# Optimization experiments

Measured on AMD Instinct MI355X. Metric: run time of the kernel, lower is better.

Reference implementation:

```python
import jax, jax.numpy as jnp
import numpy as np
import math

B, S, D, H = 4, 2048, 1024, 16
DK = D // H


def setup_inputs() -> dict:
    key = jax.random.key(0)
    ks = jax.random.split(key, 10)
    scale = 0.02
    q = jax.random.normal(ks[0], (B, S, D), jnp.float32)
    k = jax.random.normal(ks[1], (B, S, D), jnp.float32)
    v = jax.random.normal(ks[2], (B, S, D), jnp.float32)
    # additive float src_mask [S,S]: causal-style mask (0 allowed, -1e9 blocked)
    causal = jnp.tril(jnp.ones((S, S), jnp.float32))
    src_mask = jnp.where(causal > 0, 0.0, -1e9).astype(jnp.float32)
    # key padding mask [B,S]: last 256 keys of each sequence are padding
    key_padding_mask = (jnp.arange(S)[None, :] >= (S - 256)) & jnp.ones((B, 1), bool)
    Wq = jax.random.normal(ks[3], (D, D), jnp.float32) * scale
    Wk = jax.random.normal(ks[4], (D, D), jnp.float32) * scale
    Wv = jax.random.normal(ks[5], (D, D), jnp.float32) * scale
    Wo = jax.random.normal(ks[6], (D, D), jnp.float32) * scale
    bq = jnp.zeros((D,), jnp.float32)
    bk = jnp.zeros((D,), jnp.float32)
    bv = jnp.zeros((D,), jnp.float32)
    bo = jnp.zeros((D,), jnp.float32)
    return {"q": q, "k": k, "v": v, "src_mask": src_mask,
            "key_padding_mask": key_padding_mask,
            "Wq": Wq, "bq": bq, "Wk": Wk, "bk": bk,
            "Wv": Wv, "bv": bv, "Wo": Wo, "bo": bo}


def reference(q, k, v, src_mask, key_padding_mask, Wq, bq, Wk, bk, Wv, bv, Wo, bo):
    bs = q.shape[0]
    # torch Linear: x @ W.T + b
    qh = (q @ Wq.T + bq).reshape(bs, -1, H, DK).transpose(0, 2, 1, 3)  # [B,H,S,dk]
    kh = (k @ Wk.T + bk).reshape(bs, -1, H, DK).transpose(0, 2, 1, 3)
    vh = (v @ Wv.T + bv).reshape(bs, -1, H, DK).transpose(0, 2, 1, 3)
    scores = jnp.einsum('bhqd,bhkd->bhqk', qh, kh) / math.sqrt(DK)
    # float additive src_mask: scores += mask[None, None]
    scores = scores + src_mask[None, None, :, :]
    # boolean key padding mask: fill masked keys with -inf
    scores = jnp.where(key_padding_mask[:, None, None, :], -jnp.inf, scores)
    attn = jax.nn.softmax(scores, axis=-1)  # dropout inactive (eval / p=0)
    out = jnp.einsum('bhqk,bhkd->bhqd', attn, vh)
    concat = out.transpose(0, 2, 1, 3).reshape(bs, -1, D)
    return concat @ Wo.T + bo
```

## Files before the change

### kernel.cpp

```cpp
#include <hip/hip_runtime.h>
#include <hip/hip_bf16.h>
#include <stdint.h>

#define S_LEN 2048
#define DMODEL 1024
#define DKH 64
#define KV_ALLOWED 1792
#define QSCALE 0.18033688011112042f

typedef __attribute__((ext_vector_type(4))) float f32x4;
typedef __attribute__((ext_vector_type(8))) short bf16x8;
typedef __attribute__((ext_vector_type(8))) unsigned short u16x8;
typedef __attribute__((ext_vector_type(4))) unsigned short u16x4;

static __device__ __forceinline__ float fast_exp2(float x) {
    return __builtin_amdgcn_exp2f(x);
}
static __device__ __forceinline__ unsigned short f2bf(float f) {
    __hip_bfloat16 h = __float2bfloat16(f);
    union { __hip_bfloat16 h; unsigned short u; } c; c.h = h; return c.u;
}
static __device__ __forceinline__ float bf2f(unsigned short b) {
    union { unsigned u; float f; } c; c.u = ((unsigned)b) << 16; return c.f;
}
static __device__ __forceinline__ u16x8 cvt2x4(const float4 a, const float4 b) {
    u16x8 r;
    r[0] = f2bf(a.x); r[1] = f2bf(a.y); r[2] = f2bf(a.z); r[3] = f2bf(a.w);
    r[4] = f2bf(b.x); r[5] = f2bf(b.y); r[6] = f2bf(b.z); r[7] = f2bf(b.w);
    return r;
}

#define BAR_LGKM() do { \
    asm volatile("s_waitcnt lgkmcnt(0)" ::: "memory"); \
    __builtin_amdgcn_s_barrier(); \
    __builtin_amdgcn_sched_barrier(0); \
} while (0)

#define A_OFF(buf) ((buf) * 8192)
#define B_OFF(buf) (16384 + (buf) * 16384)

__global__ __launch_bounds__(256) void cvt_w(
        const float* __restrict__ w0, const float* __restrict__ w1,
        const float* __restrict__ w2, const float* __restrict__ w3,
        unsigned short* __restrict__ out) {
    const float* src = (blockIdx.y == 0) ? w0 : (blockIdx.y == 1) ? w1
                     : (blockIdx.y == 2) ? w2 : w3;
    unsigned short* dst = out + (size_t)blockIdx.y * 1048576;
    const int i = (blockIdx.x * 256 + threadIdx.x) * 16;
    float4 f0 = *(const float4*)(src + i);
    float4 f1 = *(const float4*)(src + i + 4);
    float4 f2 = *(const float4*)(src + i + 8);
    float4 f3 = *(const float4*)(src + i + 12);
    *(u16x8*)(dst + i)     = cvt2x4(f0, f1);
    *(u16x8*)(dst + i + 8) = cvt2x4(f2, f3);
}

template<int OUT_MODE>
__global__ __launch_bounds__(512) void gemm_proj(
        const float* __restrict__ A, const unsigned short* __restrict__ Bw,
        const float* __restrict__ bias, unsigned short* __restrict__ Cout) {
    __shared__ unsigned short smem[49152];
    const int tid = threadIdx.x;
    const int lane = tid & 63, wv = tid >> 6;
    const int wr = wv >> 2, wc = wv & 3;
    const int g = lane >> 4, lo = lane & 15;
    const int wg = ((int)blockIdx.x & 7) * 32 + ((int)blockIdx.x >> 3);
    const int m0 = (wg >> 2) << 7, n0 = (wg & 3) << 8;

    const int sr = tid >> 2;
    const int sc = (tid & 3) << 4;
    const int swzA = (sr & 7) << 3;
    const int gsw = ((lane & 7) ^ (lane >> 3)) << 3;
    const int rswz = (lo & 7) << 3;

    f32x4 acc[4][4];
#pragma unroll
    for (int i = 0; i < 4; ++i)
#pragma unroll
        for (int j = 0; j < 4; ++j) acc[i][j] = (f32x4){0.f, 0.f, 0.f, 0.f};

    const float* gaBase = A + (size_t)(m0 + sr) * 1024 + sc;

    auto LOADA = [&](int ko, float4* pa) {
        const float* ga = gaBase + ko;
        pa[0] = *(const float4*)(ga);      pa[1] = *(const float4*)(ga + 4);
        pa[2] = *(const float4*)(ga + 8);  pa[3] = *(const float4*)(ga + 12);
    };
    auto WRITEA = [&](int buf, const float4* pa) {
        *(u16x8*)&smem[A_OFF(buf) + sr * 64 + ((sc + 0) ^ swzA)] = cvt2x4(pa[0], pa[1]);
        *(u16x8*)&smem[A_OFF(buf) + sr * 64 + ((sc + 8) ^ swzA)] = cvt2x4(pa[2], pa[3]);
    };
    auto LOADB = [&](int ko, u16x8* pb) {
#pragma unroll
        for (int c = 0; c < 4; ++c) {
            const int rb = c * 64 + wv * 8 + (lane >> 3);
            pb[c] = *(const u16x8*)(Bw + (size_t)(n0 + rb) * 1024 + ko + gsw);
        }
    };
    auto WRITEB = [&](int buf, const u16x8* pb) {
#pragma unroll
        for (int c = 0; c < 4; ++c) {
            const int rb = c * 64 + wv * 8 + (lane >> 3);
            *(u16x8*)&smem[B_OFF(buf) + rb * 64 + ((lane & 7) << 3)] = pb[c];
        }
    };

    float4 pa[4];
    u16x8 pb[4];
    LOADA(0, pa);  LOADB(0, pb);
    WRITEA(0, pa); WRITEB(0, pb);
    LOADA(64, pa); LOADB(64, pb);
    BAR_LGKM();

    int cur = 0;
    for (int k0 = 0; k0 < 1024; k0 += 64) {
        if (k0 + 64 < 1024) {
            WRITEA(cur ^ 1, pa);
            WRITEB(cur ^ 1, pb);
        }
        __builtin_amdgcn_sched_barrier(0);
        const int ka = (k0 + 128 < 1024) ? (k0 + 128) : 0;
        LOADA(ka, pa);
        LOADB(ka, pb);
        __builtin_amdgcn_sched_barrier(0);

#pragma unroll
        for (int kk = 0; kk < 2; ++kk) {
            bf16x8 af[4], bfr[4];
#pragma unroll
            for (int mi = 0; mi < 4; ++mi) {
                const int r = wr * 64 + mi * 16 + lo;
                af[mi] = *(const bf16x8*)&smem[A_OFF(cur) + r * 64 + ((kk * 32 + g * 8) ^ rswz)];
            }
#pragma unroll
            for (int ni = 0; ni < 4; ++ni) {
                const int r = wc * 64 + ni * 16 + lo;
                bfr[ni] = *(const bf16x8*)&smem[B_OFF(cur) + r * 64 + ((kk * 32 + g * 8) ^ rswz)];
            }
#pragma unroll
            for (int mi = 0; mi < 4; ++mi)
#pragma unroll
                for (int ni = 0; ni < 4; ++ni)
                    acc[mi][ni] = __builtin_amdgcn_mfma_f32_16x16x32_bf16(af[mi], bfr[ni], acc[mi][ni], 0, 0, 0);
        }
        BAR_LGKM();
        cur ^= 1;
    }

    if (OUT_MODE == 2) {
#pragma unroll
        for (int mi = 0; mi < 4; ++mi) {
            const int rb = wr * 64 + mi * 16 + g * 4;
#pragma unroll
            for (int ni = 0; ni < 4; ++ni) {
                const int c = wc * 64 + ni * 16 + lo;
                const float bvv = bias[n0 + c];
                u16x4 w;
#pragma unroll
                for (int j = 0; j < 4; ++j) w[j] = f2bf(acc[mi][ni][j] + bvv);
                *(u16x4*)&smem[c * 128 + (rb ^ ((c & 15) << 3))] = w;
            }
        }
        __syncthreads();
        const int c2 = tid >> 1, hf = tid & 1;
        const int bglob = m0 >> 11;
        unsigned short* vrow = Cout + (((size_t)(bglob * 1024 + n0 + c2)) << 11)
                             + (m0 & 2047) + hf * 64;
#pragma unroll
        for (int i = 0; i < 8; ++i) {
            u16x8 vv = *(const u16x8*)&smem[c2 * 128 + ((hf * 64 + i * 8) ^ ((c2 & 15) << 3))];
            *(u16x8*)(vrow + i * 8) = vv;
        }
    } else {
#pragma unroll
        for (int mi = 0; mi < 4; ++mi) {
            const int row = m0 + wr * 64 + mi * 16 + g * 4;
#pragma unroll
            for (int ni = 0; ni < 4; ++ni) {
                const int col = n0 + wc * 64 + ni * 16 + lo;
                const float bvv = bias[col];
#pragma unroll
                for (int j = 0; j < 4; ++j)
                    Cout[(size_t)(row + j) * 1024 + col] = f2bf(acc[mi][ni][j] + bvv);
            }
        }
    }
}

__global__ __launch_bounds__(512) void gemm_out(
        const unsigned short* __restrict__ Ab, const unsigned short* __restrict__ Bw,
        const float* __restrict__ bias, float* __restrict__ Cout) {
    __shared__ unsigned short smem[49152];
    const int tid = threadIdx.x;
    const int lane = tid & 63, wv = tid >> 6;
    const int wr = wv >> 2, wc = wv & 3;
    const int g = lane >> 4, lo = lane & 15;
    const int wg = ((int)blockIdx.x & 7) * 32 + ((int)blockIdx.x >> 3);
    const int m0 = (wg >> 2) << 7, n0 = (wg & 3) << 8;
    const int gsw = ((lane & 7) ^ (lane >> 3)) << 3;
    const int rswz = (lo & 7) << 3;

    f32x4 acc[4][4];
#pragma unroll
    for (int i = 0; i < 4; ++i)
#pragma unroll
        for (int j = 0; j < 4; ++j) acc[i][j] = (f32x4){0.f, 0.f, 0.f, 0.f};

    auto LOADAB = [&](int ko, u16x8* pa, u16x8* pb) {
#pragma unroll
        for (int c = 0; c < 2; ++c) {
            const int rb = c * 64 + wv * 8 + (lane >> 3);
            pa[c] = *(const u16x8*)(Ab + (size_t)(m0 + rb) * 1024 + ko + gsw);
        }
#pragma unroll
        for (int c = 0; c < 4; ++c) {
            const int rb = c * 64 + wv * 8 + (lane >> 3);
            pb[c] = *(const u16x8*)(Bw + (size_t)(n0 + rb) * 1024 + ko + gsw);
        }
    };
    auto WRITEAB = [&](int buf, const u16x8* pa, const u16x8* pb) {
#pragma unroll
        for (int c = 0; c < 2; ++c) {
            const int rb = c * 64 + wv * 8 + (lane >> 3);
            *(u16x8*)&smem[A_OFF(buf) + rb * 64 + ((lane & 7) << 3)] = pa[c];
        }
#pragma unroll
        for (int c = 0; c < 4; ++c) {
            const int rb = c * 64 + wv * 8 + (lane >> 3);
            *(u16x8*)&smem[B_OFF(buf) + rb * 64 + ((lane & 7) << 3)] = pb[c];
        }
    };

    u16x8 pa[2], pb[4];
    LOADAB(0, pa, pb);
    WRITEAB(0, pa, pb);
    LOADAB(64, pa, pb);
    BAR_LGKM();

    int cur = 0;
    for (int k0 = 0; k0 < 1024; k0 += 64) {
        if (k0 + 64 < 1024) WRITEAB(cur ^ 1, pa, pb);
        __builtin_amdgcn_sched_barrier(0);
        const int ka = (k0 + 128 < 1024) ? (k0 + 128) : 0;
        LOADAB(ka, pa, pb);
        __builtin_amdgcn_sched_barrier(0);

#pragma unroll
        for (int kk = 0; kk < 2; ++kk) {
            bf16x8 af[4], bfr[4];
#pragma unroll
            for (int mi = 0; mi < 4; ++mi) {
                const int r = wr * 64 + mi * 16 + lo;
                af[mi] = *(const bf16x8*)&smem[A_OFF(cur) + r * 64 + ((kk * 32 + g * 8) ^ rswz)];
            }
#pragma unroll
            for (int ni = 0; ni < 4; ++ni) {
                const int r = wc * 64 + ni * 16 + lo;
                bfr[ni] = *(const bf16x8*)&smem[B_OFF(cur) + r * 64 + ((kk * 32 + g * 8) ^ rswz)];
            }
#pragma unroll
            for (int mi = 0; mi < 4; ++mi)
#pragma unroll
                for (int ni = 0; ni < 4; ++ni)
                    acc[mi][ni] = __builtin_amdgcn_mfma_f32_16x16x32_bf16(af[mi], bfr[ni], acc[mi][ni], 0, 0, 0);
        }
        BAR_LGKM();
        cur ^= 1;
    }

#pragma unroll
    for (int mi = 0; mi < 4; ++mi) {
        const int row = m0 + wr * 64 + mi * 16 + g * 4;
#pragma unroll
        for (int ni = 0; ni < 4; ++ni) {
            const int col = n0 + wc * 64 + ni * 16 + lo;
            const float bvv = bias[col];
#pragma unroll
            for (int j = 0; j < 4; ++j)
                Cout[(size_t)(row + j) * 1024 + col] = acc[mi][ni][j] + bvv;
        }
    }
}

__global__ __launch_bounds__(512) void attn_fwd(
        unsigned short* __restrict__ QO, const unsigned short* __restrict__ Kh,
        const unsigned short* __restrict__ Vt) {
    __shared__ unsigned short K_lds[64 * 72];
    __shared__ unsigned short Vt_lds[64 * 68];
    __shared__ unsigned short P_lds[8][16 * 68];

    const int bh = blockIdx.x;
    const int b = bh >> 4, h = bh & 15;
    const int yy = blockIdx.y;
    const int tid = threadIdx.x, lane = tid & 63, wv = tid >> 6;
    const int g = lane >> 4, lo = lane & 15;
    const int str = tid >> 3;
    const int stc = (tid & 7) << 3;

    const unsigned short* kbase = Kh + ((size_t)b * S_LEN + str) * DMODEL + h * DKH + stc;
    const unsigned short* vbase = Vt + ((size_t)(bh * 64 + str)) * S_LEN + stc;

    const int ytile = (wv < 4) ? (31 - yy) : yy;
    const int qw0 = (ytile << 6) + ((wv & 3) << 4);
    const int qrow = qw0 + lo;
    const int lastk = (qrow < KV_ALLOWED - 1) ? qrow : (KV_ALLOWED - 1);
    const int wmin_last = (qw0 < KV_ALLOWED - 1) ? qw0 : (KV_ALLOWED - 1);
    const int wave_last_k = (qw0 + 15 < KV_ALLOWED - 1) ? (qw0 + 15) : (KV_ALLOWED - 1);

    const int nt_long = (32 - yy < 28) ? (32 - yy) : 28;

    bf16x8 qf[2];
#pragma unroll
    for (int kk = 0; kk < 2; ++kk) {
        const u16x8 raw = *(const u16x8*)(QO + ((size_t)b * S_LEN + qrow) * DMODEL
                                          + h * DKH + kk * 32 + g * 8);
        bf16x8 sc16;
#pragma unroll
        for (int e = 0; e < 8; ++e) sc16[e] = (short)f2bf(bf2f(raw[e]) * QSCALE);
        qf[kk] = sc16;
    }

    float l_part = 0.f;
    f32x4 o_acc[4];
#pragma unroll
    for (int nf = 0; nf < 4; ++nf) o_acc[nf] = (f32x4){0.f, 0.f, 0.f, 0.f};

    u16x8 cK = *(const u16x8*)kbase;
    u16x8 cV = *(const u16x8*)vbase;

    for (int t = 0; t < nt_long; ++t) {
        const int kv0 = t << 6;
        __syncthreads();
        *(u16x8*)&K_lds[str * 72 + stc] = cK;
        *(u16x8*)&Vt_lds[str * 68 + stc] = cV;
        __syncthreads();
        if (t + 1 < nt_long) {
            cK = *(const u16x8*)(kbase + (size_t)(kv0 + 64) * DMODEL);
            cV = *(const u16x8*)(vbase + kv0 + 64);
        }

        if (kv0 <= wave_last_k) {
            f32x4 sacc[4];
#pragma unroll
            for (int nf = 0; nf < 4; ++nf) sacc[nf] = (f32x4){0.f, 0.f, 0.f, 0.f};
            __builtin_amdgcn_s_setprio(1);
#pragma unroll
            for (int kk = 0; kk < 2; ++kk) {
                bf16x8 kf[4];
#pragma unroll
                for (int nf = 0; nf < 4; ++nf)
                    kf[nf] = *(const bf16x8*)&K_lds[(nf * 16 + lo) * 72 + kk * 32 + g * 8];
#pragma unroll
                for (int nf = 0; nf < 4; ++nf)
                    sacc[nf] = __builtin_amdgcn_mfma_f32_16x16x32_bf16(kf[nf], qf[kk], sacc[nf], 0, 0, 0);
            }
            __builtin_amdgcn_s_setprio(0);

            if (kv0 + 63 > wmin_last) {
#pragma unroll
                for (int nf = 0; nf < 4; ++nf)
#pragma unroll
                    for (int j = 0; j < 4; ++j) {
                        const int col = kv0 + nf * 16 + g * 4 + j;
                        sacc[nf][j] = (col <= lastk) ? sacc[nf][j] : -__builtin_inff();
                    }
            }

            float ps[4];
#pragma unroll
            for (int nf = 0; nf < 4; ++nf) {
#pragma unroll
                for (int j = 0; j < 4; ++j)
                    sacc[nf][j] = fast_exp2(sacc[nf][j]);
                ps[nf] = (sacc[nf][0] + sacc[nf][1]) + (sacc[nf][2] + sacc[nf][3]);
            }
            l_part += (ps[0] + ps[1]) + (ps[2] + ps[3]);

#pragma unroll
            for (int nf = 0; nf < 4; ++nf) {
                u16x4 pk;
#pragma unroll
                for (int j = 0; j < 4; ++j) pk[j] = f2bf(sacc[nf][j]);
                *(u16x4*)&P_lds[wv][lo * 68 + nf * 16 + g * 4] = pk;
            }

            __builtin_amdgcn_s_setprio(1);
#pragma unroll
            for (int kk = 0; kk < 2; ++kk) {
                const bf16x8 pf = *(const bf16x8*)&P_lds[wv][lo * 68 + kk * 32 + g * 8];
                bf16x8 vf[4];
#pragma unroll
                for (int nf = 0; nf < 4; ++nf)
                    vf[nf] = *(const bf16x8*)&Vt_lds[(nf * 16 + lo) * 68 + kk * 32 + g * 8];
#pragma unroll
                for (int nf = 0; nf < 4; ++nf)
                    o_acc[nf] = __builtin_amdgcn_mfma_f32_16x16x32_bf16(vf[nf], pf, o_acc[nf], 0, 0, 0);
            }
            __builtin_amdgcn_s_setprio(0);
        }
    }

    float l_run = l_part + __shfl_xor(l_part, 16, 64);
    l_run += __shfl_xor(l_run, 32, 64);

    const float rl = 1.0f / l_run;
    unsigned short* orow = QO + ((size_t)b * S_LEN + qrow) * DMODEL + h * DKH;
#pragma unroll
    for (int nf = 0; nf < 4; ++nf) {
        u16x4 ok;
#pragma unroll
        for (int j = 0; j < 4; ++j) ok[j] = f2bf(o_acc[nf][j] * rl);
        *(u16x4*)(orow + nf * 16 + g * 4) = ok;
    }
}

extern "C" void kernel_launch(void* const* d_in, const int* in_sizes, int n_in,
                              void* d_out, int out_size, void* d_ws, size_t ws_size,
                              hipStream_t stream) {
    const float* q  = (const float*)d_in[0];
    const float* k  = (const float*)d_in[1];
    const float* v  = (const float*)d_in[2];
    const float* Wq = (const float*)d_in[5];
    const float* bq = (const float*)d_in[6];
    const float* Wk = (const float*)d_in[7];
    const float* bk = (const float*)d_in[8];
    const float* Wv = (const float*)d_in[9];
    const float* bv = (const float*)d_in[10];
    const float* Wo = (const float*)d_in[11];
    const float* bo = (const float*)d_in[12];

    unsigned short* ws = (unsigned short*)d_ws;
    unsigned short* qh = ws;
    unsigned short* kh = ws + 8388608;
    unsigned short* vt = ws + 16777216;
    unsigned short* Wb = ws + 25165824;

    cvt_w<<<dim3(256, 4), dim3(256), 0, stream>>>(Wq, Wk, Wv, Wo, Wb);

    gemm_proj<0><<<256, dim3(512), 0, stream>>>(q, Wb,           bq, qh);
    gemm_proj<0><<<256, dim3(512), 0, stream>>>(k, Wb + 1048576, bk, kh);
    gemm_proj<2><<<256, dim3(512), 0, stream>>>(v, Wb + 2097152, bv, vt);

    attn_fwd<<<dim3(64, 16), dim3(512), 0, stream>>>(qh, kh, vt);

    gemm_out<<<256, dim3(512), 0, stream>>>(qh, Wb + 3145728, bo, (float*)d_out);
}
```

Before: 172.4 us.

## Have each attention wave process two query tiles to reuse K/V fragments

The attention kernel drops from 8 waves to 4 waves per block. Each wave now handles both the long (31-yy) and short (yy) query tiles, sharing the K and V fragments it reads from LDS across the two. Staging loads double per thread to keep the 64x64 tiles filled. This halves LDS fragment reads per MFMA, but it raises register pressure and leaves fewer waves per block to hide latency.

New measurement: 188.9 us. 1.1x slower.

```diff
diff --git a/kernel.cpp b/kernel.cpp
--- a/kernel.cpp
+++ b/kernel.cpp
@@ -282,67 +282,90 @@
     }
 }
 
-__global__ __launch_bounds__(512) void attn_fwd(
+__global__ __launch_bounds__(256) void attn_fwd(
         unsigned short* __restrict__ QO, const unsigned short* __restrict__ Kh,
         const unsigned short* __restrict__ Vt) {
     __shared__ unsigned short K_lds[64 * 72];
     __shared__ unsigned short Vt_lds[64 * 68];
-    __shared__ unsigned short P_lds[8][16 * 68];
+    __shared__ unsigned short P_lds[4][2][16 * 68];
 
     const int bh = blockIdx.x;
     const int b = bh >> 4, h = bh & 15;
     const int yy = blockIdx.y;
     const int tid = threadIdx.x, lane = tid & 63, wv = tid >> 6;
     const int g = lane >> 4, lo = lane & 15;
-    const int str = tid >> 3;
-    const int stc = (tid & 7) << 3;
+    const int str = tid >> 2;
+    const int stc = (tid & 3) << 4;
 
     const unsigned short* kbase = Kh + ((size_t)b * S_LEN + str) * DMODEL + h * DKH + stc;
     const unsigned short* vbase = Vt + ((size_t)(bh * 64 + str)) * S_LEN + stc;
 
-    const int ytile = (wv < 4) ? (31 - yy) : yy;
-    const int qw0 = (ytile << 6) + ((wv & 3) << 4);
-    const int qrow = qw0 + lo;
-    const int lastk = (qrow < KV_ALLOWED - 1) ? qrow : (KV_ALLOWED - 1);
-    const int wmin_last = (qw0 < KV_ALLOWED - 1) ? qw0 : (KV_ALLOWED - 1);
-    const int wave_last_k = (qw0 + 15 < KV_ALLOWED - 1) ? (qw0 + 15) : (KV_ALLOWED - 1);
+    const int ytA = 31 - yy, ytB = yy;
+    const int qw0A = (ytA << 6) + (wv << 4);
+    const int qw0B = (ytB << 6) + (wv << 4);
+    const int qrowA = qw0A + lo, qrowB = qw0B + lo;
+    const int lastkA = (qrowA < KV_ALLOWED - 1) ? qrowA : (KV_ALLOWED - 1);
+    const int lastkB = (qrowB < KV_ALLOWED - 1) ? qrowB : (KV_ALLOWED - 1);
+    const int wminA = (qw0A < KV_ALLOWED - 1) ? qw0A : (KV_ALLOWED - 1);
+    const int wminB = (qw0B < KV_ALLOWED - 1) ? qw0B : (KV_ALLOWED - 1);
+    const int wlkA = (qw0A + 15 < KV_ALLOWED - 1) ? (qw0A + 15) : (KV_ALLOWED - 1);
+    const int wlkB = (qw0B + 15 < KV_ALLOWED - 1) ? (qw0B + 15) : (KV_ALLOWED - 1);
 
     const int nt_long = (32 - yy < 28) ? (32 - yy) : 28;
 
-    bf16x8 qf[2];
+    bf16x8 qfA[2], qfB[2];
 #pragma unroll
     for (int kk = 0; kk < 2; ++kk) {
-        const u16x8 raw = *(const u16x8*)(QO + ((size_t)b * S_LEN + qrow) * DMODEL
-                                          + h * DKH + kk * 32 + g * 8);
-        bf16x8 sc16;
-#pragma unroll
-        for (int e = 0; e < 8; ++e) sc16[e] = (short)f2bf(bf2f(raw[e]) * QSCALE);
-        qf[kk] = sc16;
-    }
-
-    float l_part = 0.f;
-    f32x4 o_acc[4];
-#pragma unroll
-    for (int nf = 0; nf < 4; ++nf) o_acc[nf] = (f32x4){0.f, 0.f, 0.f, 0.f};
-
-    u16x8 cK = *(const u16x8*)kbase;
-    u16x8 cV = *(const u16x8*)vbase;
+        const u16x8 rawA = *(const u16x8*)(QO + ((size_t)b * S_LEN + qrowA) * DMODEL
+                                           + h * DKH + kk * 32 + g * 8);
+        const u16x8 rawB = *(const u16x8*)(QO + ((size_t)b * S_LEN + qrowB) * DMODEL
+                                           + h * DKH + kk * 32 + g * 8);
+        bf16x8 sA, sB;
+#pragma unroll
+        for (int e = 0; e < 8; ++e) {
+            sA[e] = (short)f2bf(bf2f(rawA[e]) * QSCALE);
+            sB[e] = (short)f2bf(bf2f(rawB[e]) * QSCALE);
+        }
+        qfA[kk] = sA; qfB[kk] = sB;
+    }
+
+    float lpA = 0.f, lpB = 0.f;
+    f32x4 oA[4], oB[4];
+#pragma unroll
+    for (int nf = 0; nf < 4; ++nf) {
+        oA[nf] = (f32x4){0.f, 0.f, 0.f, 0.f};
+        oB[nf] = (f32x4){0.f, 0.f, 0.f, 0.f};
+    }
+
+    u16x8 cK0 = *(const u16x8*)kbase;
+    u16x8 cK1 = *(const u16x8*)(kbase + 8);
+    u16x8 cV0 = *(const u16x8*)vbase;
+    u16x8 cV1 = *(const u16x8*)(vbase + 8);
 
     for (int t = 0; t < nt_long; ++t) {
         const int kv0 = t << 6;
         __syncthreads();
-        *(u16x8*)&K_lds[str * 72 + stc] = cK;
-        *(u16x8*)&Vt_lds[str * 68 + stc] = cV;
+        *(u16x8*)&K_lds[str * 72 + stc] = cK0;
+        *(u16x8*)&K_lds[str * 72 + stc + 8] = cK1;
+        *(u16x8*)&Vt_lds[str * 68 + stc] = cV0;
+        *(u16x8*)&Vt_lds[str * 68 + stc + 8] = cV1;
         __syncthreads();
         if (t + 1 < nt_long) {
-            cK = *(const u16x8*)(kbase + (size_t)(kv0 + 64) * DMODEL);
-            cV = *(const u16x8*)(vbase + kv0 + 64);
-        }
-
-        if (kv0 <= wave_last_k) {
-            f32x4 sacc[4];
-#pragma unroll
-            for (int nf = 0; nf < 4; ++nf) sacc[nf] = (f32x4){0.f, 0.f, 0.f, 0.f};
+            cK0 = *(const u16x8*)(kbase + (size_t)(kv0 + 64) * DMODEL);
+            cK1 = *(const u16x8*)(kbase + (size_t)(kv0 + 64) * DMODEL + 8);
+            cV0 = *(const u16x8*)(vbase + kv0 + 64);
+            cV1 = *(const u16x8*)(vbase + kv0 + 64 + 8);
+        }
+
+        if (kv0 <= wlkA) {
+            const bool actB = (kv0 <= wlkB);
+
+            f32x4 sA[4], sB[4];
+#pragma unroll
+            for (int nf = 0; nf < 4; ++nf) {
+                sA[nf] = (f32x4){0.f, 0.f, 0.f, 0.f};
+                sB[nf] = (f32x4){0.f, 0.f, 0.f, 0.f};
+            }
             __builtin_amdgcn_s_setprio(1);
 #pragma unroll
             for (int kk = 0; kk < 2; ++kk) {
@@ -352,65 +375,113 @@
                     kf[nf] = *(const bf16x8*)&K_lds[(nf * 16 + lo) * 72 + kk * 32 + g * 8];
 #pragma unroll
                 for (int nf = 0; nf < 4; ++nf)
-                    sacc[nf] = __builtin_amdgcn_mfma_f32_16x16x32_bf16(kf[nf], qf[kk], sacc[nf], 0, 0, 0);
+                    sA[nf] = __builtin_amdgcn_mfma_f32_16x16x32_bf16(kf[nf], qfA[kk], sA[nf], 0, 0, 0);
+                if (actB) {
+#pragma unroll
+                    for (int nf = 0; nf < 4; ++nf)
+                        sB[nf] = __builtin_amdgcn_mfma_f32_16x16x32_bf16(kf[nf], qfB[kk], sB[nf], 0, 0, 0);
+                }
             }
             __builtin_amdgcn_s_setprio(0);
 
-            if (kv0 + 63 > wmin_last) {
+            if (kv0 + 63 > wminA) {
 #pragma unroll
                 for (int nf = 0; nf < 4; ++nf)
 #pragma unroll
                     for (int j = 0; j < 4; ++j) {
                         const int col = kv0 + nf * 16 + g * 4 + j;
-                        sacc[nf][j] = (col <= lastk) ? sacc[nf][j] : -__builtin_inff();
+                        sA[nf][j] = (col <= lastkA) ? sA[nf][j] : -__builtin_inff();
                     }
             }
-
-            float ps[4];
-#pragma unroll
-            for (int nf = 0; nf < 4; ++nf) {
-#pragma unroll
-                for (int j = 0; j < 4; ++j)
-                    sacc[nf][j] = fast_exp2(sacc[nf][j]);
-                ps[nf] = (sacc[nf][0] + sacc[nf][1]) + (sacc[nf][2] + sacc[nf][3]);
-            }
-            l_part += (ps[0] + ps[1]) + (ps[2] + ps[3]);
-
-#pragma unroll
-            for (int nf = 0; nf < 4; ++nf) {
-                u16x4 pk;
-#pragma unroll
-                for (int j = 0; j < 4; ++j) pk[j] = f2bf(sacc[nf][j]);
-                *(u16x4*)&P_lds[wv][lo * 68 + nf * 16 + g * 4] = pk;
+            {
+                float ps[4];
+#pragma unroll
+                for (int nf = 0; nf < 4; ++nf) {
+#pragma unroll
+                    for (int j = 0; j < 4; ++j) sA[nf][j] = fast_exp2(sA[nf][j]);
+                    ps[nf] = (sA[nf][0] + sA[nf][1]) + (sA[nf][2] + sA[nf][3]);
+                }
+                lpA += (ps[0] + ps[1]) + (ps[2] + ps[3]);
+#pragma unroll
+                for (int nf = 0; nf < 4; ++nf) {
+                    u16x4 pk;
+#pragma unroll
+                    for (int j = 0; j < 4; ++j) pk[j] = f2bf(sA[nf][j]);
+                    *(u16x4*)&P_lds[wv][0][lo * 68 + nf * 16 + g * 4] = pk;
+                }
+            }
+
+            if (actB) {
+                if (kv0 + 63 > wminB) {
+#pragma unroll
+                    for (int nf = 0; nf < 4; ++nf)
+#pragma unroll
+                        for (int j = 0; j < 4; ++j) {
+                            const int col = kv0 + nf * 16 + g * 4 + j;
+                            sB[nf][j] = (col <= lastkB) ? sB[nf][j] : -__builtin_inff();
+                        }
+                }
+                float ps[4];
+#pragma unroll
+                for (int nf = 0; nf < 4; ++nf) {
+#pragma unroll
+                    for (int j = 0; j < 4; ++j) sB[nf][j] = fast_exp2(sB[nf][j]);
+                    ps[nf] = (sB[nf][0] + sB[nf][1]) + (sB[nf][2] + sB[nf][3]);
+                }
+                lpB += (ps[0] + ps[1]) + (ps[2] + ps[3]);
+#pragma unroll
+                for (int nf = 0; nf < 4; ++nf) {
+                    u16x4 pk;
+#pragma unroll
+                    for (int j = 0; j < 4; ++j) pk[j] = f2bf(sB[nf][j]);
+                    *(u16x4*)&P_lds[wv][1][lo * 68 + nf * 16 + g * 4] = pk;
+                }
             }
 
             __builtin_amdgcn_s_setprio(1);
 #pragma unroll
             for (int kk = 0; kk < 2; ++kk) {
-                const bf16x8 pf = *(const bf16x8*)&P_lds[wv][lo * 68 + kk * 32 + g * 8];
                 bf16x8 vf[4];
 #pragma unroll
                 for (int nf = 0; nf < 4; ++nf)
                     vf[nf] = *(const bf16x8*)&Vt_lds[(nf * 16 + lo) * 68 + kk * 32 + g * 8];
+                const bf16x8 pfA = *(const bf16x8*)&P_lds[wv][0][lo * 68 + kk * 32 + g * 8];
 #pragma unroll
                 for (int nf = 0; nf < 4; ++nf)
-                    o_acc[nf] = __builtin_amdgcn_mfma_f32_16x16x32_bf16(vf[nf], pf, o_acc[nf], 0, 0, 0);
+                    oA[nf] = __builtin_amdgcn_mfma_f32_16x16x32_bf16(vf[nf], pfA, oA[nf], 0, 0, 0);
+                if (actB) {
+                    const bf16x8 pfB = *(const bf16x8*)&P_lds[wv][1][lo * 68 + kk * 32 + g * 8];
+#pragma unroll
+                    for (int nf = 0; nf < 4; ++nf)
+                        oB[nf] = __builtin_amdgcn_mfma_f32_16x16x32_bf16(vf[nf], pfB, oB[nf], 0, 0, 0);
+                }
             }
             __builtin_amdgcn_s_setprio(0);
         }
     }
 
-    float l_run = l_part + __shfl_xor(l_part, 16, 64);
-    l_run += __shfl_xor(l_run, 32, 64);
-
-    const float rl = 1.0f / l_run;
-    unsigned short* orow = QO + ((size_t)b * S_LEN + qrow) * DMODEL + h * DKH;
+    float lA = lpA + __shfl_xor(lpA, 16, 64);
+    lA += __shfl_xor(lA, 32, 64);
+    float lB = lpB + __shfl_xor(lpB, 16, 64);
+    lB += __shfl_xor(lB, 32, 64);
+
+    const float rlA = 1.0f / lA;
+    unsigned short* orowA = QO + ((size_t)b * S_LEN + qrowA) * DMODEL + h * DKH;
 #pragma unroll
     for (int nf = 0; nf < 4; ++nf) {
         u16x4 ok;
 #pragma unroll
-        for (int j = 0; j < 4; ++j) ok[j] = f2bf(o_acc[nf][j] * rl);
-        *(u16x4*)(orow + nf * 16 + g * 4) = ok;
+        for (int j = 0; j < 4; ++j) ok[j] = f2bf(oA[nf][j] * rlA);
+        *(u16x4*)(orowA + nf * 16 + g * 4) = ok;
+    }
+    const float rlB = 1.0f / lB;
+    unsigned short* orowB = QO + ((size_t)b * S_LEN + qrowB) * DMODEL + h * DKH;
+#pragma unroll
+    for (int nf = 0; nf < 4; ++nf) {
+        u16x4 ok;
+#pragma unroll
+        for (int j = 0; j < 4; ++j) ok[j] = f2bf(oB[nf][j] * rlB);
+        *(u16x4*)(orowB + nf * 16 + g * 4) = ok;
     }
 }
 
@@ -441,7 +512,7 @@
     gemm_proj<0><<<256, dim3(512), 0, stream>>>(k, Wb + 1048576, bk, kh);
     gemm_proj<2><<<256, dim3(512), 0, stream>>>(v, Wb + 2097152, bv, vt);
 
-    attn_fwd<<<dim3(64, 16), dim3(512), 0, stream>>>(qh, kh, vt);
+    attn_fwd<<<dim3(64, 16), dim3(256), 0, stream>>>(qh, kh, vt);
 
     gemm_out<<<256, dim3(512), 0, stream>>>(qh, Wb + 3145728, bo, (float*)d_out);
 }
```
